# Kernel tuning notes

Measured on AMD Instinct MI355X. Metric: run time of the kernel, lower is better.

## Reference

```python
import jax, jax.numpy as jnp
import numpy as np

N_NODES = 100000
N_EDGES = 3200000
N_GRAPHS = 256
D_IN = 320
D_H = 64


def setup_inputs() -> dict:
    key = jax.random.key(0)
    ks = jax.random.split(key, 8)
    x = jax.random.normal(ks[0], (N_NODES, D_IN), dtype=jnp.float32)
    edge_index = jax.random.randint(ks[1], (2, N_EDGES), 0, N_NODES, dtype=jnp.int64)
    batch = jnp.sort(jax.random.randint(ks[2], (N_NODES,), 0, N_GRAPHS, dtype=jnp.int64))
    # Glorot-ish init for weights
    W1 = jax.random.normal(ks[3], (D_IN, D_H), dtype=jnp.float32) / np.sqrt(D_IN)
    W2 = jax.random.normal(ks[4], (D_H, D_H), dtype=jnp.float32) / np.sqrt(D_H)
    W3 = jax.random.normal(ks[5], (D_H, D_H), dtype=jnp.float32) / np.sqrt(D_H)
    Wl = jax.random.normal(ks[6], (D_H, 1), dtype=jnp.float32) / np.sqrt(D_H)
    return {
        "x": x, "edge_index": edge_index, "batch": batch,
        "W1": W1, "b1": jnp.zeros((D_H,), jnp.float32),
        "W2": W2, "b2": jnp.zeros((D_H,), jnp.float32),
        "W3": W3, "b3": jnp.zeros((D_H,), jnp.float32),
        "Wl": Wl, "bl": jnp.zeros((1,), jnp.float32),
    }


def _gcn_norm(edge_index, n_nodes):
    # PyG GCNConv default: add self-loops, symmetric normalization D^-1/2 (A+I) D^-1/2
    loops = jnp.arange(n_nodes, dtype=edge_index.dtype)
    src = jnp.concatenate([edge_index[0], loops])  # [E+N]
    dst = jnp.concatenate([edge_index[1], loops])  # [E+N]
    deg = jax.ops.segment_sum(jnp.ones_like(dst, dtype=jnp.float32), dst,
                              num_segments=n_nodes)
    dinv = jnp.where(deg > 0, jax.lax.rsqrt(deg), 0.0)
    norm = dinv[src] * dinv[dst]  # [E+N]
    return src, dst, norm


def _gcn_conv(h, W, b, src, dst, norm, n_nodes):
    h = h @ W                                   # [N, d_out] transform first (PyG order)
    msg = h[src] * norm[:, None]                # gather + scale, [E+N, d_out]
    agg = jax.ops.segment_sum(msg, dst, num_segments=n_nodes)  # scatter-add
    return agg + b


def reference(x, edge_index, batch, W1, b1, W2, b2, W3, b3, Wl, bl):
    n = x.shape[0]
    src, dst, norm = _gcn_norm(edge_index, n)
    h = jax.nn.relu(_gcn_conv(x, W1, b1, src, dst, norm, n))
    h = jax.nn.relu(_gcn_conv(h, W2, b2, src, dst, norm, n))
    h = _gcn_conv(h, W3, b3, src, dst, norm, n)
    # global_mean_pool over batch ids
    sums = jax.ops.segment_sum(h, batch, num_segments=N_GRAPHS)       # [G, d]
    cnts = jax.ops.segment_sum(jnp.ones((n,), jnp.float32), batch,
                               num_segments=N_GRAPHS)                  # [G]
    pooled = sums / jnp.maximum(cnts, 1.0)[:, None]
    # dropout is identity at inference (p=0.5, training=False)
    return pooled @ Wl + bl                                            # [G, 1]
```

## Files before the change

kernel.cpp:

```cpp
#include <hip/hip_runtime.h>
#include <hip/hip_bf16.h>
#include <hip/hip_fp16.h>

#define N_NODES 100000
#define N_EDGES 3200000
#define N_GRAPHS 256
#define D_IN 320
#define D_H 64

#define NBIN 391
#define BIN_CAP 14336
#define HIST_BLOCKS 256
#define HIST_CHUNK ((N_EDGES + HIST_BLOCKS - 1) / HIST_BLOCKS)
#define PART_BLOCKS 200
#define PART_CHUNK ((N_EDGES + PART_BLOCKS - 1) / PART_BLOCKS)
#define COLB_CAP 5500000


__global__ __launch_bounds__(256) void k_hist(const int* __restrict__ dst,
                                              int* __restrict__ ghist) {
    __shared__ int lh[NBIN];
    for (int i = threadIdx.x; i < NBIN; i += 256) lh[i] = 0;
    __syncthreads();
    int beg = blockIdx.x * HIST_CHUNK;
    int end = min(beg + HIST_CHUNK, N_EDGES);
    for (int e = beg + threadIdx.x; e < end; e += 256)
        atomicAdd(&lh[dst[e] >> 8], 1);
    __syncthreads();
    for (int i = threadIdx.x; i < NBIN; i += 256)
        if (lh[i]) atomicAdd(&ghist[i], lh[i]);
}

__global__ __launch_bounds__(512) void k_scanbins(const int* __restrict__ ghist,
                                                  int* __restrict__ binbase,
                                                  int* __restrict__ gcur) {
    __shared__ int sa[512], sb[512];
    int t = threadIdx.x;
    int v = (t < NBIN) ? ghist[t] : 0;
    sa[t] = v;
    __syncthreads();
    int* in = sa; int* out = sb;
    for (int off = 1; off < 512; off <<= 1) {
        out[t] = in[t] + (t >= off ? in[t - off] : 0);
        __syncthreads();
        int* tmp = in; in = out; out = tmp;
    }
    int excl = in[t] - v;
    if (t < NBIN) { binbase[t] = excl; gcur[t] = excl; }
    if (t == 511) binbase[NBIN] = in[511];
}

__global__ __launch_bounds__(256) void k_part(const int* __restrict__ src,
                                              const int* __restrict__ dst,
                                              int* __restrict__ gcur,
                                              int* __restrict__ ebuf) {
    __shared__ int lh[NBIN], gb[NBIN], cur[NBIN];
    for (int i = threadIdx.x; i < NBIN; i += 256) { lh[i] = 0; cur[i] = 0; }
    __syncthreads();
    int beg = blockIdx.x * PART_CHUNK;
    int end = min(beg + PART_CHUNK, N_EDGES);
    for (int e = beg + threadIdx.x; e < end; e += 256)
        atomicAdd(&lh[dst[e] >> 8], 1);
    __syncthreads();
    for (int i = threadIdx.x; i < NBIN; i += 256)
        gb[i] = lh[i] ? atomicAdd(&gcur[i], lh[i]) : 0;
    __syncthreads();
    for (int e = beg + threadIdx.x; e < end; e += 256) {
        int d = dst[e], s = src[e];
        int bin = d >> 8;
        int r = atomicAdd(&cur[bin], 1);
        ebuf[gb[bin] + r] = ((d & 255) << 17) | s;
    }
}

__global__ __launch_bounds__(256) void k_binpad(const int* __restrict__ binbase,
                                                const int* __restrict__ ebuf,
                                                int* __restrict__ pbin,
                                                int* __restrict__ lofs,
                                                float* __restrict__ dinv) {
    __shared__ int hc[256], sa[256], sb[256];
    int b = blockIdx.x, t = threadIdx.x;
    int e0 = binbase[b], e1 = binbase[b + 1];
    hc[t] = 0;
    __syncthreads();
    for (int i = e0 + t; i < e1; i += 256)
        atomicAdd(&hc[ebuf[i] >> 17], 1);
    __syncthreads();
    int deg = hc[t];
    int pdeg = (deg + 31) & ~31;
    sa[t] = pdeg;
    __syncthreads();
    int* in = sa; int* out = sb;
    for (int o = 1; o < 256; o <<= 1) {
        out[t] = in[t] + (t >= o ? in[t - o] : 0);
        __syncthreads();
        int* tm = in; in = out; out = tm;
    }
    int excl = in[t] - pdeg;
    lofs[(b << 8) + t] = excl;
    int node = (b << 8) + t;
    if (node < N_NODES) dinv[node] = rsqrtf((float)(deg + 1));
    if (t == 255) pbin[b] = in[255];
}

__global__ __launch_bounds__(512) void k_scanp(const int* __restrict__ pbin,
                                               int* __restrict__ pbinbase,
                                               int* __restrict__ prowptr,
                                               __half* __restrict__ u) {
    __shared__ int sa[512], sb[512];
    int t = threadIdx.x;
    int v = (t < NBIN) ? pbin[t] : 0;
    sa[t] = v;
    __syncthreads();
    int* in = sa; int* out = sb;
    for (int off = 1; off < 512; off <<= 1) {
        out[t] = in[t] + (t >= off ? in[t - off] : 0);
        __syncthreads();
        int* tmp = in; in = out; out = tmp;
    }
    int excl = in[t] - v;
    if (t < NBIN) pbinbase[t] = excl;
    if (t == 511) { pbinbase[NBIN] = in[511]; prowptr[N_NODES] = in[511]; }
    if (t < 32) ((unsigned*)(u + (size_t)N_NODES * D_H))[t] = 0u;
}

__global__ __launch_bounds__(256) void k_sortbin(const int* __restrict__ binbase,
                                                 const int* __restrict__ pbinbase,
                                                 const int* __restrict__ lofs,
                                                 const int* __restrict__ ebuf,
                                                 int* __restrict__ col,
                                                 int* __restrict__ prowptr) {
    __shared__ int hc[256], sc[256];
    __shared__ int scol[BIN_CAP];
    int b = blockIdx.x, t = threadIdx.x;
    int d0 = b << 8;
    int e0 = binbase[b], e1 = binbase[b + 1];
    int pb0 = pbinbase[b], pb1 = pbinbase[b + 1];
    hc[t] = 0;
    __syncthreads();
    for (int i = e0 + t; i < e1; i += 256)
        atomicAdd(&hc[ebuf[i] >> 17], 1);
    __syncthreads();
    int lb = lofs[d0 + t];
    int deg = hc[t];
    int pdeg = (deg + 31) & ~31;
    sc[t] = lb;
    int node = d0 + t;
    if (node < N_NODES) prowptr[node] = pb0 + lb;
    __syncthreads();
    for (int i = e0 + t; i < e1; i += 256) {
        int pk = ebuf[i];
        int p = atomicAdd(&sc[pk >> 17], 1);
        if (p < BIN_CAP) scol[p] = pk & 0x1FFFF;
    }
    __syncthreads();
    for (int j = lb + deg; j < lb + pdeg; ++j)
        if (j < BIN_CAP) scol[j] = N_NODES;
    __syncthreads();
    int n = pb1 - pb0;
    for (int i = t; i < n; i += 256) col[pb0 + i] = scol[i];
}


template<int K>
__global__ __launch_bounds__(256) void k_gemm(const float* __restrict__ A,
                                              const float* __restrict__ W,
                                              const float* __restrict__ dinv,
                                              __half* __restrict__ u) {
    __shared__ float xt[32][64];
    __shared__ float ws[32][64];
    int t = threadIdx.x;
    int ti = t & 15;
    int tj = t >> 4;
    int node0 = blockIdx.x * 64;
    float acc[4][4] = {{0.f}};

    for (int kc = 0; kc < K; kc += 32) {
        if (kc) __syncthreads();
#pragma unroll
        for (int hh = 0; hh < 2; ++hh) {
            int f = t + 256 * hh;
            int m = f >> 3, c = f & 7;
            int node = node0 + m;
            if (node >= N_NODES) node = N_NODES - 1;
            float4 v = *(const float4*)(A + (size_t)node * K + kc + 4 * c);
            int cs = (m + 4 * c) & 63;
            xt[4 * c + 0][cs] = v.x;
            xt[4 * c + 1][cs] = v.y;
            xt[4 * c + 2][cs] = v.z;
            xt[4 * c + 3][cs] = v.w;
            int kw = f >> 4, cw = f & 15;
            *(float4*)&ws[kw][4 * cw] =
                *(const float4*)(W + (size_t)(kc + kw) * D_H + 4 * cw);
        }
        __syncthreads();
#pragma unroll
        for (int k = 0; k < 32; ++k) {
            float4 xv = *(const float4*)&xt[k][(4 * tj + 4 * (k >> 2)) & 63];
            float4 wv = *(const float4*)&ws[k][4 * ti];
            float xa[4] = {xv.x, xv.y, xv.z, xv.w};
            float wa[4] = {wv.x, wv.y, wv.z, wv.w};
#pragma unroll
            for (int i = 0; i < 4; ++i)
#pragma unroll
                for (int j = 0; j < 4; ++j)
                    acc[i][j] = fmaf(xa[i], wa[j], acc[i][j]);
        }
    }
#pragma unroll
    for (int i = 0; i < 4; ++i) {
        int node = node0 + 4 * tj + i;
        if (node < N_NODES) {
            float dv = dinv[node];
            __half2* up = (__half2*)(u + (size_t)node * D_H + 4 * ti);
            up[0] = __floats2half2_rn(acc[i][0] * dv, acc[i][1] * dv);
            up[1] = __floats2half2_rn(acc[i][2] * dv, acc[i][3] * dv);
        }
    }
}

__global__ __launch_bounds__(256) void k_gemm_h(const __half* __restrict__ A,
                                                const float* __restrict__ W,
                                                const float* __restrict__ dinv,
                                                __half* __restrict__ u) {
    __shared__ float xt[32][64];
    __shared__ float ws[32][64];
    int t = threadIdx.x;
    int ti = t & 15;
    int tj = t >> 4;
    int node0 = blockIdx.x * 64;
    float acc[4][4] = {{0.f}};

    for (int kc = 0; kc < 64; kc += 32) {
        if (kc) __syncthreads();
#pragma unroll
        for (int hh = 0; hh < 2; ++hh) {
            int f = t + 256 * hh;
            int m = f >> 3, c = f & 7;
            int node = node0 + m;
            if (node >= N_NODES) node = N_NODES - 1;
            uint2 v = *(const uint2*)(A + (size_t)node * D_H + kc + 4 * c);
            __half2 h0 = *reinterpret_cast<__half2*>(&v.x);
            __half2 h1 = *reinterpret_cast<__half2*>(&v.y);
            float2 f0 = __half22float2(h0);
            float2 f1 = __half22float2(h1);
            int cs = (m + 4 * c) & 63;
            xt[4 * c + 0][cs] = f0.x;
            xt[4 * c + 1][cs] = f0.y;
            xt[4 * c + 2][cs] = f1.x;
            xt[4 * c + 3][cs] = f1.y;
            int kw = f >> 4, cw = f & 15;
            *(float4*)&ws[kw][4 * cw] =
                *(const float4*)(W + (size_t)(kc + kw) * D_H + 4 * cw);
        }
        __syncthreads();
#pragma unroll
        for (int k = 0; k < 32; ++k) {
            float4 xv = *(const float4*)&xt[k][(4 * tj + 4 * (k >> 2)) & 63];
            float4 wv = *(const float4*)&ws[k][4 * ti];
            float xa[4] = {xv.x, xv.y, xv.z, xv.w};
            float wa[4] = {wv.x, wv.y, wv.z, wv.w};
#pragma unroll
            for (int i = 0; i < 4; ++i)
#pragma unroll
                for (int j = 0; j < 4; ++j)
                    acc[i][j] = fmaf(xa[i], wa[j], acc[i][j]);
        }
    }
#pragma unroll
    for (int i = 0; i < 4; ++i) {
        int node = node0 + 4 * tj + i;
        if (node < N_NODES) {
            float dv = dinv[node];
            __half2* up = (__half2*)(u + (size_t)node * D_H + 4 * ti);
            up[0] = __floats2half2_rn(acc[i][0] * dv, acc[i][1] * dv);
            up[1] = __floats2half2_rn(acc[i][2] * dv, acc[i][3] * dv);
        }
    }
}


__device__ __forceinline__ void acc4(float4& a, uint2 w) {
    __half2 h0 = *reinterpret_cast<__half2*>(&w.x);
    __half2 h1 = *reinterpret_cast<__half2*>(&w.y);
    float2 f0 = __half22float2(h0);
    float2 f1 = __half22float2(h1);
    a.x += f0.x; a.y += f0.y; a.z += f1.x; a.w += f1.y;
}

__device__ __forceinline__ float4 agg_gather4(const __half* __restrict__ u,
                                              const int* __restrict__ col,
                                              int beg, int end, int q, int fq) {
    float4 acc = make_float4(0.f, 0.f, 0.f, 0.f);
    int base = beg;
    for (; base + 31 < end; base += 32) {
        int e = base + q;
        int s0 = col[e],      s1 = col[e + 4],  s2 = col[e + 8],  s3 = col[e + 12];
        int s4 = col[e + 16], s5 = col[e + 20], s6 = col[e + 24], s7 = col[e + 28];
        uint2 w0 = *(const uint2*)(u + (size_t)s0 * D_H + fq * 4);
        uint2 w1 = *(const uint2*)(u + (size_t)s1 * D_H + fq * 4);
        uint2 w2 = *(const uint2*)(u + (size_t)s2 * D_H + fq * 4);
        uint2 w3 = *(const uint2*)(u + (size_t)s3 * D_H + fq * 4);
        uint2 w4 = *(const uint2*)(u + (size_t)s4 * D_H + fq * 4);
        uint2 w5 = *(const uint2*)(u + (size_t)s5 * D_H + fq * 4);
        uint2 w6 = *(const uint2*)(u + (size_t)s6 * D_H + fq * 4);
        uint2 w7 = *(const uint2*)(u + (size_t)s7 * D_H + fq * 4);
        acc4(acc, w0); acc4(acc, w1); acc4(acc, w2); acc4(acc, w3);
        acc4(acc, w4); acc4(acc, w5); acc4(acc, w6); acc4(acc, w7);
    }
    for (int e = base + q; e < end; e += 4) {
        uint2 w = *(const uint2*)(u + (size_t)col[e] * D_H + fq * 4);
        acc4(acc, w);
    }
    return acc;
}

__global__ __launch_bounds__(256) void k_agg(const __half* __restrict__ u,
                                             const int* __restrict__ prowptr,
                                             const int* __restrict__ col,
                                             const float* __restrict__ dinv,
                                             const float* __restrict__ b,
                                             __half* __restrict__ h) {
    int t = threadIdx.x;
    int lane = t & 63, q = lane >> 4, fq = lane & 15;
    int node = (blockIdx.x * blockDim.x + t) >> 6;
    if (node >= N_NODES) return;
    float4 acc = agg_gather4(u, col, prowptr[node], prowptr[node + 1], q, fq);
    if (q == 0) {
        uint2 w = *(const uint2*)(u + (size_t)node * D_H + fq * 4);
        acc4(acc, w);
    }
    acc.x += __shfl_xor(acc.x, 16, 64); acc.y += __shfl_xor(acc.y, 16, 64);
    acc.z += __shfl_xor(acc.z, 16, 64); acc.w += __shfl_xor(acc.w, 16, 64);
    acc.x += __shfl_xor(acc.x, 32, 64); acc.y += __shfl_xor(acc.y, 32, 64);
    acc.z += __shfl_xor(acc.z, 32, 64); acc.w += __shfl_xor(acc.w, 32, 64);
    if (q == 0) {
        float dv = dinv[node];
        float4 bb = *(const float4*)(b + 4 * fq);
        uint2 o;
        __half2 o0 = __floats2half2_rn(fmaxf(acc.x * dv + bb.x, 0.f),
                                       fmaxf(acc.y * dv + bb.y, 0.f));
        __half2 o1 = __floats2half2_rn(fmaxf(acc.z * dv + bb.z, 0.f),
                                       fmaxf(acc.w * dv + bb.w, 0.f));
        o.x = *reinterpret_cast<unsigned*>(&o0);
        o.y = *reinterpret_cast<unsigned*>(&o1);
        *(uint2*)(h + (size_t)node * D_H + 4 * fq) = o;
    }
}

__global__ __launch_bounds__(256) void k_agg_dot(const __half* __restrict__ uin,
                                                 const int* __restrict__ prowptr,
                                                 const int* __restrict__ col,
                                                 const float* __restrict__ dinv,
                                                 const float* __restrict__ b,
                                                 const float* __restrict__ Wl,
                                                 float* __restrict__ val) {
    int t = threadIdx.x;
    int lane = t & 63, q = lane >> 4, fq = lane & 15;
    int node = (blockIdx.x * blockDim.x + t) >> 6;
    if (node >= N_NODES) return;
    float4 acc = agg_gather4(uin, col, prowptr[node], prowptr[node + 1], q, fq);
    if (q == 0) {
        uint2 w = *(const uint2*)(uin + (size_t)node * D_H + fq * 4);
        acc4(acc, w);
    }
    float4 wl = *(const float4*)(Wl + 4 * fq);
    float dv = dinv[node];
    float v = dv * (acc.x * wl.x + acc.y * wl.y + acc.z * wl.z + acc.w * wl.w);
    if (q == 0) {
        float4 bb = *(const float4*)(b + 4 * fq);
        v += bb.x * wl.x + bb.y * wl.y + bb.z * wl.z + bb.w * wl.w;
    }
#pragma unroll
    for (int m = 32; m > 0; m >>= 1) v += __shfl_xor(v, m, 64);
    if (lane == 0) val[node] = v;
}

__global__ __launch_bounds__(256) void k_gpool(const float* __restrict__ val,
                                               const int* __restrict__ batch,
                                               const float* __restrict__ bl,
                                               float* __restrict__ out) {
    int g = blockIdx.x;
    int l = 0, r = N_NODES;
    while (l < r) { int m = (l + r) >> 1; if (batch[m] < g) l = m + 1; else r = m; }
    int lo = l;
    r = N_NODES;
    while (l < r) { int m = (l + r) >> 1; if (batch[m] < g + 1) l = m + 1; else r = m; }
    int hi = l;
    float s = 0.0f;
    for (int i = lo + threadIdx.x; i < hi; i += 256) s += val[i];
#pragma unroll
    for (int m = 32; m > 0; m >>= 1) s += __shfl_xor(s, m, 64);
    __shared__ float red[4];
    int wid = threadIdx.x >> 6, lane = threadIdx.x & 63;
    if (lane == 0) red[wid] = s;
    __syncthreads();
    if (threadIdx.x == 0) {
        float t = red[0] + red[1] + red[2] + red[3];
        out[g] = t / fmaxf((float)(hi - lo), 1.0f) + bl[0];
    }
}


extern "C" void kernel_launch(void* const* d_in, const int* in_sizes, int n_in,
                              void* d_out, int out_size, void* d_ws, size_t ws_size,
                              hipStream_t stream) {
    const float* x   = (const float*)d_in[0];
    const int*   ei  = (const int*)d_in[1];
    const int*   bat = (const int*)d_in[2];
    const float* W1  = (const float*)d_in[3];
    const float* b1  = (const float*)d_in[4];
    const float* W2  = (const float*)d_in[5];
    const float* b2  = (const float*)d_in[6];
    const float* W3  = (const float*)d_in[7];
    const float* b3  = (const float*)d_in[8];
    const float* Wl  = (const float*)d_in[9];
    const float* bl  = (const float*)d_in[10];
    float* out = (float*)d_out;

    char* p = (char*)d_ws;
    auto alloc = [&](size_t bytes) -> void* {
        void* r = (void*)p;
        p += (bytes + 255) & ~(size_t)255;
        return r;
    };
    int*    ghist    = (int*)alloc((size_t)NBIN * 4);
    int*    binbase  = (int*)alloc((size_t)(NBIN + 1) * 4);
    int*    gcur     = (int*)alloc((size_t)NBIN * 4);
    int*    pbin     = (int*)alloc((size_t)NBIN * 4);
    int*    pbinbase = (int*)alloc((size_t)(NBIN + 1) * 4);
    int*    lofs     = (int*)alloc((size_t)NBIN * 256 * 4);
    int*    prowptr  = (int*)alloc((size_t)(N_NODES + 1) * 4);
    float*  dinv     = (float*)alloc((size_t)N_NODES * 4);
    int*    colb     = (int*)alloc((size_t)COLB_CAP * 4);
    int*    ebuf     = (int*)alloc((size_t)N_EDGES * 4);
    __half* u        = (__half*)alloc((size_t)(N_NODES + 1) * D_H * 2);
    __half* h        = (__half*)alloc((size_t)N_NODES * D_H * 2);
    float*  val      = (float*)alloc((size_t)N_NODES * 4);

    hipMemsetAsync(ghist, 0, (size_t)NBIN * 4, stream);

    const int* srcp = ei;
    const int* dstp = ei + N_EDGES;

    int wbl = (N_NODES * 64 + 255) / 256;
    int gbl = (N_NODES + 63) / 64;

    k_hist<<<HIST_BLOCKS, 256, 0, stream>>>(dstp, ghist);
    k_scanbins<<<1, 512, 0, stream>>>(ghist, binbase, gcur);
    k_part<<<PART_BLOCKS, 256, 0, stream>>>(srcp, dstp, gcur, ebuf);
    k_binpad<<<NBIN, 256, 0, stream>>>(binbase, ebuf, pbin, lofs, dinv);
    k_scanp<<<1, 512, 0, stream>>>(pbin, pbinbase, prowptr, u);
    k_sortbin<<<NBIN, 256, 0, stream>>>(binbase, pbinbase, lofs, ebuf, colb, prowptr);

    k_gemm<D_IN><<<gbl, 256, 0, stream>>>(x, W1, dinv, u);
    k_agg<<<wbl, 256, 0, stream>>>(u, prowptr, colb, dinv, b1, h);
    k_gemm_h<<<gbl, 256, 0, stream>>>(h, W2, dinv, u);
    k_agg<<<wbl, 256, 0, stream>>>(u, prowptr, colb, dinv, b2, h);
    k_gemm_h<<<gbl, 256, 0, stream>>>(h, W3, dinv, u);
    k_agg_dot<<<wbl, 256, 0, stream>>>(u, prowptr, colb, dinv, b3, Wl, val);

    k_gpool<<<N_GRAPHS, 256, 0, stream>>>(val, bat, bl, out);
}
```

Before: 389.4 us.

## Collapse third GCN layer into scalar aggregation via precomputed W3·Wl projection

Since the final layer's output is only used through a dot product with Wl, the code precomputes W3·Wl and b3·Wl. The second-layer aggregation then emits one scalar per node instead of a 64-wide fp16 row, and the third layer aggregates scalars instead of 64-wide features. This removes the third dense GEMM and a full 64-wide gather pass. Separately, the degree is packed into lofs so k_sortbin no longer recomputes the per-bin histogram with shared atomics. The trade-off is fp32 scalar reassociation and a degree field capped by the bit packing.

Measured after the change: 335.3 us (median of 2 runs). 13.9% less time.

```diff
diff --git a/kernel.cpp b/kernel.cpp
--- a/kernel.cpp
+++ b/kernel.cpp
@@ -97,7 +97,7 @@
         int* tm = in; in = out; out = tm;
     }
     int excl = in[t] - pdeg;
-    lofs[(b << 8) + t] = excl;
+    lofs[(b << 8) + t] = excl | (deg << 14);
     int node = (b << 8) + t;
     if (node < N_NODES) dinv[node] = rsqrtf((float)(deg + 1));
     if (t == 255) pbin[b] = in[255];
@@ -106,7 +106,8 @@
 __global__ __launch_bounds__(512) void k_scanp(const int* __restrict__ pbin,
                                                int* __restrict__ pbinbase,
                                                int* __restrict__ prowptr,
-                                               __half* __restrict__ u) {
+                                               __half* __restrict__ u,
+                                               float* __restrict__ z) {
     __shared__ int sa[512], sb[512];
     int t = threadIdx.x;
     int v = (t < NBIN) ? pbin[t] : 0;
@@ -122,6 +123,7 @@
     if (t < NBIN) pbinbase[t] = excl;
     if (t == 511) { pbinbase[NBIN] = in[511]; prowptr[N_NODES] = in[511]; }
     if (t < 32) ((unsigned*)(u + (size_t)N_NODES * D_H))[t] = 0u;
+    if (t == 32) z[N_NODES] = 0.f;
 }
 
 __global__ __launch_bounds__(256) void k_sortbin(const int* __restrict__ binbase,
@@ -130,19 +132,15 @@
                                                  const int* __restrict__ ebuf,
                                                  int* __restrict__ col,
                                                  int* __restrict__ prowptr) {
-    __shared__ int hc[256], sc[256];
+    __shared__ int sc[256];
     __shared__ int scol[BIN_CAP];
     int b = blockIdx.x, t = threadIdx.x;
     int d0 = b << 8;
     int e0 = binbase[b], e1 = binbase[b + 1];
     int pb0 = pbinbase[b], pb1 = pbinbase[b + 1];
-    hc[t] = 0;
-    __syncthreads();
-    for (int i = e0 + t; i < e1; i += 256)
-        atomicAdd(&hc[ebuf[i] >> 17], 1);
-    __syncthreads();
-    int lb = lofs[d0 + t];
-    int deg = hc[t];
+    int lv = lofs[d0 + t];
+    int lb = lv & 0x3FFF;
+    int deg = lv >> 14;
     int pdeg = (deg + 31) & ~31;
     sc[t] = lb;
     int node = d0 + t;
@@ -159,6 +157,19 @@
     __syncthreads();
     int n = pb1 - pb0;
     for (int i = t; i < n; i += 256) col[pb0 + i] = scol[i];
+}
+
+__global__ void k_w3l(const float* __restrict__ W3, const float* __restrict__ Wl,
+                      const float* __restrict__ b3, float* __restrict__ w3lb) {
+    int k = threadIdx.x;
+    float s = 0.f;
+#pragma unroll
+    for (int j = 0; j < 64; ++j) s = fmaf(W3[k * 64 + j], Wl[j], s);
+    w3lb[k] = s;
+    float bs = b3[k] * Wl[k];
+#pragma unroll
+    for (int m = 32; m > 0; m >>= 1) bs += __shfl_xor(bs, m, 64);
+    if (k == 0) w3lb[64] = bs;
 }
 
 
@@ -348,32 +359,55 @@
     }
 }
 
-__global__ __launch_bounds__(256) void k_agg_dot(const __half* __restrict__ uin,
-                                                 const int* __restrict__ prowptr,
-                                                 const int* __restrict__ col,
-                                                 const float* __restrict__ dinv,
-                                                 const float* __restrict__ b,
-                                                 const float* __restrict__ Wl,
-                                                 float* __restrict__ val) {
+__global__ __launch_bounds__(256) void k_agg_z(const __half* __restrict__ u,
+                                               const int* __restrict__ prowptr,
+                                               const int* __restrict__ col,
+                                               const float* __restrict__ dinv,
+                                               const float* __restrict__ b,
+                                               const float* __restrict__ w3lb,
+                                               float* __restrict__ z) {
     int t = threadIdx.x;
     int lane = t & 63, q = lane >> 4, fq = lane & 15;
     int node = (blockIdx.x * blockDim.x + t) >> 6;
     if (node >= N_NODES) return;
-    float4 acc = agg_gather4(uin, col, prowptr[node], prowptr[node + 1], q, fq);
+    float4 acc = agg_gather4(u, col, prowptr[node], prowptr[node + 1], q, fq);
     if (q == 0) {
-        uint2 w = *(const uint2*)(uin + (size_t)node * D_H + fq * 4);
+        uint2 w = *(const uint2*)(u + (size_t)node * D_H + fq * 4);
         acc4(acc, w);
     }
-    float4 wl = *(const float4*)(Wl + 4 * fq);
+    acc.x += __shfl_xor(acc.x, 16, 64); acc.y += __shfl_xor(acc.y, 16, 64);
+    acc.z += __shfl_xor(acc.z, 16, 64); acc.w += __shfl_xor(acc.w, 16, 64);
+    acc.x += __shfl_xor(acc.x, 32, 64); acc.y += __shfl_xor(acc.y, 32, 64);
+    acc.z += __shfl_xor(acc.z, 32, 64); acc.w += __shfl_xor(acc.w, 32, 64);
     float dv = dinv[node];
-    float v = dv * (acc.x * wl.x + acc.y * wl.y + acc.z * wl.z + acc.w * wl.w);
-    if (q == 0) {
-        float4 bb = *(const float4*)(b + 4 * fq);
-        v += bb.x * wl.x + bb.y * wl.y + bb.z * wl.z + bb.w * wl.w;
-    }
-#pragma unroll
-    for (int m = 32; m > 0; m >>= 1) v += __shfl_xor(v, m, 64);
-    if (lane == 0) val[node] = v;
+    float4 bb = *(const float4*)(b + 4 * fq);
+    float4 wv = *(const float4*)(w3lb + 4 * fq);
+    float h0 = fmaxf(acc.x * dv + bb.x, 0.f);
+    float h1 = fmaxf(acc.y * dv + bb.y, 0.f);
+    float h2v = fmaxf(acc.z * dv + bb.z, 0.f);
+    float h3v = fmaxf(acc.w * dv + bb.w, 0.f);
+    float s = h0 * wv.x + h1 * wv.y + h2v * wv.z + h3v * wv.w;
+#pragma unroll
+    for (int m = 8; m > 0; m >>= 1) s += __shfl_xor(s, m, 64);
+    if (lane == 0) z[node] = s * dv;
+}
+
+__global__ __launch_bounds__(256) void k_aggz(const float* __restrict__ z,
+                                              const int* __restrict__ prowptr,
+                                              const int* __restrict__ col,
+                                              const float* __restrict__ dinv,
+                                              const float* __restrict__ w3lb,
+                                              float* __restrict__ val) {
+    int t = threadIdx.x;
+    int lane = t & 63;
+    int node = (blockIdx.x * blockDim.x + t) >> 6;
+    if (node >= N_NODES) return;
+    int beg = prowptr[node], end = prowptr[node + 1];
+    float a = 0.f;
+    for (int e = beg + lane; e < end; e += 64) a += z[col[e]];
+#pragma unroll
+    for (int m = 32; m > 0; m >>= 1) a += __shfl_xor(a, m, 64);
+    if (lane == 0) val[node] = dinv[node] * (a + z[node]) + w3lb[64];
 }
 
 __global__ __launch_bounds__(256) void k_gpool(const float* __restrict__ val,
@@ -436,6 +470,8 @@
     int*    ebuf     = (int*)alloc((size_t)N_EDGES * 4);
     __half* u        = (__half*)alloc((size_t)(N_NODES + 1) * D_H * 2);
     __half* h        = (__half*)alloc((size_t)N_NODES * D_H * 2);
+    float*  z        = (float*)alloc((size_t)(N_NODES + 1) * 4);
+    float*  w3lb     = (float*)alloc((size_t)256);
     float*  val      = (float*)alloc((size_t)N_NODES * 4);
 
     hipMemsetAsync(ghist, 0, (size_t)NBIN * 4, stream);
@@ -450,15 +486,15 @@
     k_scanbins<<<1, 512, 0, stream>>>(ghist, binbase, gcur);
     k_part<<<PART_BLOCKS, 256, 0, stream>>>(srcp, dstp, gcur, ebuf);
     k_binpad<<<NBIN, 256, 0, stream>>>(binbase, ebuf, pbin, lofs, dinv);
-    k_scanp<<<1, 512, 0, stream>>>(pbin, pbinbase, prowptr, u);
+    k_scanp<<<1, 512, 0, stream>>>(pbin, pbinbase, prowptr, u, z);
     k_sortbin<<<NBIN, 256, 0, stream>>>(binbase, pbinbase, lofs, ebuf, colb, prowptr);
+    k_w3l<<<1, 64, 0, stream>>>(W3, Wl, b3, w3lb);
 
     k_gemm<D_IN><<<gbl, 256, 0, stream>>>(x, W1, dinv, u);
     k_agg<<<wbl, 256, 0, stream>>>(u, prowptr, colb, dinv, b1, h);
     k_gemm_h<<<gbl, 256, 0, stream>>>(h, W2, dinv, u);
-    k_agg<<<wbl, 256, 0, stream>>>(u, prowptr, colb, dinv, b2, h);
-    k_gemm_h<<<gbl, 256, 0, stream>>>(h, W3, dinv, u);
-    k_agg_dot<<<wbl, 256, 0, stream>>>(u, prowptr, colb, dinv, b3, Wl, val);
+    k_agg_z<<<wbl, 256, 0, stream>>>(u, prowptr, colb, dinv, b2, w3lb, z);
+    k_aggz<<<wbl, 256, 0, stream>>>(z, prowptr, colb, dinv, w3lb, val);
 
     k_gpool<<<N_GRAPHS, 256, 0, stream>>>(val, bat, bl, out);
 }
```
